# Performance work log

Hardware: AMD Instinct MI355X
Metric: run time of the kernel (lower is better)

## Reference

```python
import jax, jax.numpy as jnp
import numpy as np

B, N, E = 1024, 156, 1564
C_IN, C_HID, C_OUT = 301, 128, 128
BN_EPS = 1e-5


def setup_inputs() -> dict:
    key = jax.random.key(0)
    ks = jax.random.split(key, 12)
    x = jax.random.normal(ks[0], (B, N, C_IN), dtype=jnp.float32)
    edge_index = jax.random.randint(ks[1], (2, E), 0, N, dtype=jnp.int64)
    # GCNConv linear weights (PyG lin has no bias; conv bias added after aggregation)
    W0 = jax.random.normal(ks[2], (C_IN, C_HID), dtype=jnp.float32) / np.sqrt(C_IN)
    b0 = jnp.zeros((C_HID,), dtype=jnp.float32)
    W1 = jax.random.normal(ks[3], (C_HID, C_HID), dtype=jnp.float32) / np.sqrt(C_HID)
    b1 = jnp.zeros((C_HID,), dtype=jnp.float32)
    W2 = jax.random.normal(ks[4], (C_HID, C_OUT), dtype=jnp.float32) / np.sqrt(C_HID)
    b2 = jnp.zeros((C_OUT,), dtype=jnp.float32)
    # BatchNorm affine params (eval mode: running_mean=0, running_var=1)
    bn_w0 = jax.random.uniform(ks[5], (C_HID,), dtype=jnp.float32, minval=0.5, maxval=1.5)
    bn_b0 = jax.random.normal(ks[6], (C_HID,), dtype=jnp.float32) * 0.1
    bn_w1 = jax.random.uniform(ks[7], (C_HID,), dtype=jnp.float32, minval=0.5, maxval=1.5)
    bn_b1 = jax.random.normal(ks[8], (C_HID,), dtype=jnp.float32) * 0.1
    return {"x": x, "edge_index": edge_index,
            "W0": W0, "b0": b0, "bn_w0": bn_w0, "bn_b0": bn_b0,
            "W1": W1, "b1": b1, "bn_w1": bn_w1, "bn_b1": bn_b1,
            "W2": W2, "b2": b2}


def _gcn_norm(edge_index, num_nodes):
    # add self-loops, compute symmetric normalization deg^-1/2[src]*deg^-1/2[dst]
    loops = jnp.tile(jnp.arange(num_nodes, dtype=edge_index.dtype)[None, :], (2, 1))
    ei = jnp.concatenate([edge_index, loops], axis=1)  # [2, E+N]
    row, col = ei[0], ei[1]
    deg = jnp.zeros((num_nodes,), dtype=jnp.float32).at[col].add(1.0)
    dinv = jnp.where(deg > 0, deg ** -0.5, 0.0)
    return row, col, dinv[row] * dinv[col]


def _gcn_conv(h, row, col, norm, W, b):
    # h: [B, N, Cin] -> [B, N, Cout]
    h = jnp.einsum('bnc,co->bno', h, W)
    msg = h[:, row, :] * norm[None, :, None]          # [B, E+N, Cout]
    out = jnp.zeros_like(h).at[:, col, :].add(msg)    # scatter-add to dst nodes
    return out + b


def _bn_eval(h, w, b):
    # eval-mode BatchNorm1d with running_mean=0, running_var=1
    return h * (w / jnp.sqrt(1.0 + BN_EPS)) + b


def reference(x, edge_index, W0, b0, bn_w0, bn_b0, W1, b1, bn_w1, bn_b1, W2, b2):
    n = x.shape[1]
    row, col, norm = _gcn_norm(edge_index, n)
    h = jax.nn.relu(_bn_eval(_gcn_conv(x, row, col, norm, W0, b0), bn_w0, bn_b0))
    h = jax.nn.relu(_bn_eval(_gcn_conv(h, row, col, norm, W1, b1), bn_w1, bn_b1))
    return _gcn_conv(h, row, col, norm, W2, b2)
```

## Files before the change

### kernel.cpp

```cpp
#include <hip/hip_runtime.h>

#define NN    156
#define NP    160
#define CN    128
#define K0    301
#define KP0   320
#define BATCH 1024

#define W0_OFF 0
#define W1_OFF (128 * KP0)
#define W2_OFF (128 * KP0 + 128 * 128)

typedef __attribute__((ext_vector_type(8))) short bf16x8;
typedef __attribute__((ext_vector_type(4))) float f32x4;

__device__ __align__(16) ushort g_WtH[128 * (KP0 + 128 + 128)];
__device__ __align__(16) ushort g_WtL[128 * (KP0 + 128 + 128)];
__device__ __align__(16) ushort g_AdjH[NP * NP];
__device__ __align__(16) ushort g_AdjL[NP * NP];

__device__ __forceinline__ ushort bf16_rne(float f) {
    union { float f; uint32_t u; } v; v.f = f;
    return (ushort)((v.u + 0x7FFFu + ((v.u >> 16) & 1u)) >> 16);
}
__device__ __forceinline__ float bf16_f(ushort h) {
    union { float f; uint32_t u; } v; v.u = ((uint32_t)h) << 16; return v.f;
}
__device__ __forceinline__ ushort bf16_trunc(float f) {
    union { float f; uint32_t u; } v; v.f = f;
    return (ushort)(v.u >> 16);
}

__global__ __launch_bounds__(256) void prep_kernel(const int* __restrict__ ei, int E) {
    __shared__ float adjf[NP * NP];
    __shared__ int   cnt[NP];
    __shared__ float dinv_s[NP];
    const int t = threadIdx.x;
    for (int i = t; i < NP * NP; i += 256) adjf[i] = 0.f;
    for (int n = t; n < NP; n += 256) cnt[n] = (n < NN) ? 1 : 0;
    __syncthreads();
    for (int e = t; e < E; e += 256) atomicAdd(&cnt[ei[E + e]], 1);
    __syncthreads();
    for (int n = t; n < NP; n += 256)
        dinv_s[n] = (cnt[n] > 0) ? rsqrtf((float)cnt[n]) : 0.f;
    __syncthreads();
    for (int e = t; e < E; e += 256) {
        const int r = ei[e], c = ei[E + e];
        atomicAdd(&adjf[c * NP + r], dinv_s[r] * dinv_s[c]);
    }
    for (int n = t; n < NN; n += 256)
        atomicAdd(&adjf[n * NP + n], dinv_s[n] * dinv_s[n]);
    __syncthreads();
    for (int i = t; i < NP * NP; i += 256) {
        const float v = adjf[i];
        const ushort h = bf16_rne(v);
        g_AdjH[i] = h;
        g_AdjL[i] = bf16_trunc(v - bf16_f(h));
    }
}

__global__ __launch_bounds__(256) void wt_all(const float* __restrict__ W0,
        const float* __restrict__ W1, const float* __restrict__ W2) {
    const int id = blockIdx.x * 256 + threadIdx.x;
    const float* W; int K, KP, woff, local;
    if (id < 128 * KP0)              { W = W0; K = K0;  KP = KP0; woff = W0_OFF; local = id; }
    else if (id < 128 * (KP0 + 128)) { W = W1; K = 128; KP = 128; woff = W1_OFF; local = id - 128 * KP0; }
    else                             { W = W2; K = 128; KP = 128; woff = W2_OFF; local = id - 128 * (KP0 + 128); }
    const int n = local & 127, k = local >> 7;
    const float f = (k < K) ? W[(size_t)k * CN + n] : 0.f;
    const ushort h = bf16_rne(f);
    g_WtH[woff + n * KP + k] = h;
    g_WtL[woff + n * KP + k] = bf16_trunc(f - bf16_f(h));
}

__global__ __launch_bounds__(256, 2) void fused_all(
        const float* __restrict__ x,
        const float* __restrict__ cb0, const float* __restrict__ bw0, const float* __restrict__ bb0,
        const float* __restrict__ cb1, const float* __restrict__ bw1, const float* __restrict__ bb1,
        const float* __restrict__ cb2, float* __restrict__ out) {
    __shared__ __align__(16) uint8_t smem[81920];
    uint8_t* const pH = smem;
    uint8_t* const pL = smem + 40960;

    const int t = threadIdx.x;
    const int lane = t & 63, wave = t >> 6;
    const int quad = lane >> 4, l15 = lane & 15;
    const size_t arow0 = (size_t)blockIdx.x * NN;

    f32x4 acc[10][2];
    f32x4 og[2][10];

    const int kp  = (t & 15) * 2;
    const int r0s = t >> 4;
    float sv0[10], sv1[10];

    auto stage_load = [&](int kt) {
        const int kk = kt * 32 + kp;
#pragma unroll
        for (int s = 0; s < 10; s++) {
            const int r  = r0s + s * 16;
            const int rc = (r < NN) ? r : (NN - 1);
            const size_t abase = (arow0 + rc) * (size_t)K0;
            sv0[s] = (kk < K0)     ? x[abase + kk]     : 0.f;
            sv1[s] = (kk + 1 < K0) ? x[abase + kk + 1] : 0.f;
        }
    };
    auto stage_write = [&](int buf) {
        const int segoff = buf * 10240 + (((kp >> 3) * NP) << 4) + (kp & 7) * 2;
#pragma unroll
        for (int s = 0; s < 10; s++) {
            const int r = r0s + s * 16;
            const int off = segoff + (r << 4);
            const ushort h0 = bf16_rne(sv0[s]), h1 = bf16_rne(sv1[s]);
            *(ushort2*)(pH + off) = make_ushort2(h0, h1);
            *(ushort2*)(pL + off) = make_ushort2(bf16_trunc(sv0[s] - bf16_f(h0)),
                                                 bf16_trunc(sv1[s] - bf16_f(h1)));
        }
    };

    auto gemm_l0_tile = [&](int kt, int buf) {
        bf16x8 bH[2], bL[2];
#pragma unroll
        for (int j = 0; j < 2; j++) {
            const int wi = W0_OFF + (wave * 32 + j * 16 + l15) * KP0 + kt * 32 + quad * 8;
            bH[j] = *(const bf16x8*)&g_WtH[wi];
            bL[j] = *(const bf16x8*)&g_WtL[wi];
        }
#pragma unroll
        for (int i = 0; i < 10; i++) {
            const int off = buf * 10240 + ((quad * NP + i * 16 + l15) << 4);
            const bf16x8 aH = *(const bf16x8*)(pH + off);
            const bf16x8 aL = *(const bf16x8*)(pL + off);
#pragma unroll
            for (int j = 0; j < 2; j++) {
                acc[i][j] = __builtin_amdgcn_mfma_f32_16x16x32_bf16(aH, bH[j], acc[i][j], 0, 0, 0);
                acc[i][j] = __builtin_amdgcn_mfma_f32_16x16x32_bf16(aH, bL[j], acc[i][j], 0, 0, 0);
                acc[i][j] = __builtin_amdgcn_mfma_f32_16x16x32_bf16(aL, bH[j], acc[i][j], 0, 0, 0);
            }
        }
    };

    auto gemm_h = [&](int woff) {
#pragma unroll
        for (int i = 0; i < 10; i++)
#pragma unroll
            for (int j = 0; j < 2; j++) acc[i][j] = (f32x4){0.f, 0.f, 0.f, 0.f};
        for (int kt = 0; kt < 4; kt++) {
            bf16x8 bH[2], bL[2];
#pragma unroll
            for (int j = 0; j < 2; j++) {
                const int wi = woff + (wave * 32 + j * 16 + l15) * CN + kt * 32 + quad * 8;
                bH[j] = *(const bf16x8*)&g_WtH[wi];
                bL[j] = *(const bf16x8*)&g_WtL[wi];
            }
#pragma unroll
            for (int i = 0; i < 10; i++) {
                const int off = ((kt * 4 + quad) * NP + i * 16 + l15) << 4;
                const bf16x8 aH = *(const bf16x8*)(pH + off);
                const bf16x8 aL = *(const bf16x8*)(pL + off);
#pragma unroll
                for (int j = 0; j < 2; j++) {
                    acc[i][j] = __builtin_amdgcn_mfma_f32_16x16x32_bf16(aH, bH[j], acc[i][j], 0, 0, 0);
                    acc[i][j] = __builtin_amdgcn_mfma_f32_16x16x32_bf16(aH, bL[j], acc[i][j], 0, 0, 0);
                    acc[i][j] = __builtin_amdgcn_mfma_f32_16x16x32_bf16(aL, bH[j], acc[i][j], 0, 0, 0);
                }
            }
        }
    };

    auto write_tT = [&]() {
#pragma unroll
        for (int i = 0; i < 10; i++)
#pragma unroll
            for (int j = 0; j < 2; j++) {
                const int ch = wave * 32 + j * 16 + l15;
                const int s0 = i * 16 + quad * 4;
                const int off = (((s0 >> 3) * CN + ch) << 4) + (s0 & 7) * 2;
                ushort4 hs, ls;
#pragma unroll
                for (int rg = 0; rg < 4; rg++) {
                    const float v = acc[i][j][rg];
                    const ushort h = bf16_rne(v);
                    (&hs.x)[rg] = h;
                    (&ls.x)[rg] = bf16_trunc(v - bf16_f(h));
                }
                *(ushort4*)(pH + off) = hs;
                *(ushort4*)(pL + off) = ls;
            }
    };

    auto do_agg = [&]() {
#pragma unroll
        for (int mi = 0; mi < 2; mi++)
#pragma unroll
            for (int nj = 0; nj < 10; nj++) og[mi][nj] = (f32x4){0.f, 0.f, 0.f, 0.f};
        for (int k2 = 0; k2 < 5; k2++) {
            bf16x8 tAH[2], tAL[2];
#pragma unroll
            for (int mi = 0; mi < 2; mi++) {
                const int off = ((k2 * 4 + quad) * CN + wave * 32 + mi * 16 + l15) << 4;
                tAH[mi] = *(const bf16x8*)(pH + off);
                tAL[mi] = *(const bf16x8*)(pL + off);
            }
#pragma unroll
            for (int nj = 0; nj < 10; nj++) {
                const int ai = (nj * 16 + l15) * NP + k2 * 32 + quad * 8;
                const bf16x8 gH = *(const bf16x8*)&g_AdjH[ai];
                const bf16x8 gL = *(const bf16x8*)&g_AdjL[ai];
#pragma unroll
                for (int mi = 0; mi < 2; mi++) {
                    og[mi][nj] = __builtin_amdgcn_mfma_f32_16x16x32_bf16(tAH[mi], gH, og[mi][nj], 0, 0, 0);
                    og[mi][nj] = __builtin_amdgcn_mfma_f32_16x16x32_bf16(tAH[mi], gL, og[mi][nj], 0, 0, 0);
                    og[mi][nj] = __builtin_amdgcn_mfma_f32_16x16x32_bf16(tAL[mi], gH, og[mi][nj], 0, 0, 0);
                    og[mi][nj] = __builtin_amdgcn_mfma_f32_16x16x32_bf16(tAL[mi], gL, og[mi][nj], 0, 0, 0);
                }
            }
        }
    };

    auto write_h = [&](const float* cb, const float* bw, const float* bb) {
        const float inv = rsqrtf(1.f + 1e-5f);
#pragma unroll
        for (int mi = 0; mi < 2; mi++) {
            const int c0 = wave * 32 + mi * 16 + quad * 4;
            const float4 cbv = *(const float4*)&cb[c0];
            const float4 bwv = *(const float4*)&bw[c0];
            const float4 bbv = *(const float4*)&bb[c0];
#pragma unroll
            for (int nj = 0; nj < 10; nj++) {
                const int node = nj * 16 + l15;
                const int off = (((c0 >> 3) * NP + node) << 4) + (c0 & 7) * 2;
                ushort4 hs, ls;
#pragma unroll
                for (int rg = 0; rg < 4; rg++) {
                    float v = og[mi][nj][rg] + (&cbv.x)[rg];
                    v = fmaxf(fmaf(v, (&bwv.x)[rg] * inv, (&bbv.x)[rg]), 0.f);
                    const ushort h = bf16_rne(v);
                    (&hs.x)[rg] = h;
                    (&ls.x)[rg] = bf16_trunc(v - bf16_f(h));
                }
                *(ushort4*)(pH + off) = hs;
                *(ushort4*)(pL + off) = ls;
            }
        }
    };

    auto write_out = [&](const float* cb) {
#pragma unroll
        for (int mi = 0; mi < 2; mi++) {
            const int c0 = wave * 32 + mi * 16 + quad * 4;
            const float4 cbv = *(const float4*)&cb[c0];
#pragma unroll
            for (int nj = 0; nj < 10; nj++) {
                const int node = nj * 16 + l15;
                if (node < NN) {
                    float4 o;
#pragma unroll
                    for (int rg = 0; rg < 4; rg++)
                        (&o.x)[rg] = og[mi][nj][rg] + (&cbv.x)[rg];
                    *(float4*)&out[(arow0 + node) * CN + c0] = o;
                }
            }
        }
    };

#pragma unroll
    for (int i = 0; i < 10; i++)
#pragma unroll
        for (int j = 0; j < 2; j++) acc[i][j] = (f32x4){0.f, 0.f, 0.f, 0.f};
    stage_load(0);
    stage_write(0);
    __syncthreads();
    for (int kt = 0; kt < 10; kt++) {
        if (kt < 9) stage_load(kt + 1);
        gemm_l0_tile(kt, kt & 1);
        if (kt < 9) stage_write((kt + 1) & 1);
        __syncthreads();
    }
    write_tT();
    __syncthreads();
    do_agg();
    __syncthreads();
    write_h(cb0, bw0, bb0);
    __syncthreads();
    gemm_h(W1_OFF);
    __syncthreads();
    write_tT();
    __syncthreads();
    do_agg();
    __syncthreads();
    write_h(cb1, bw1, bb1);
    __syncthreads();
    gemm_h(W2_OFF);
    __syncthreads();
    write_tT();
    __syncthreads();
    do_agg();
    write_out(cb2);
}

extern "C" void kernel_launch(void* const* d_in, const int* in_sizes, int n_in,
                              void* d_out, int out_size, void* d_ws, size_t ws_size,
                              hipStream_t stream) {
    const float* x    = (const float*)d_in[0];
    const int*   ei   = (const int*)  d_in[1];
    const float* W0   = (const float*)d_in[2];
    const float* b0   = (const float*)d_in[3];
    const float* bnw0 = (const float*)d_in[4];
    const float* bnb0 = (const float*)d_in[5];
    const float* W1   = (const float*)d_in[6];
    const float* b1   = (const float*)d_in[7];
    const float* bnw1 = (const float*)d_in[8];
    const float* bnb1 = (const float*)d_in[9];
    const float* W2   = (const float*)d_in[10];
    const float* b2   = (const float*)d_in[11];
    float* out = (float*)d_out;

    const int E = in_sizes[1] / 2;

    prep_kernel<<<1, 256, 0, stream>>>(ei, E);
    wt_all<<<288, 256, 0, stream>>>(W0, W1, W2);
    fused_all<<<BATCH, 256, 0, stream>>>(x, b0, bnw0, bnb0,
                                         b1, bnw1, bnb1, b2, out);
}
```

Before: 469.4 us.

## Split fused GCN kernel across 8 waves and drop low-low aggregation term

Doubles the block to 512 threads so each wave computes half the rows in the feature GEMMs and a 16-channel slice in the adjacency aggregation, cutting accumulator registers and raising waves per CU. The aggregation drops the lo×lo bf16 split product, reducing MFMA work at a small precision cost. The adjacency-prep and weight-split kernels are merged into one launch to remove a kernel launch. Staging loads are redistributed across the larger thread count.

```diff
diff --git a/kernel.cpp b/kernel.cpp
--- a/kernel.cpp
+++ b/kernel.cpp
@@ -31,49 +31,50 @@
     return (ushort)(v.u >> 16);
 }
 
-__global__ __launch_bounds__(256) void prep_kernel(const int* __restrict__ ei, int E) {
+__global__ __launch_bounds__(256) void prep_wt(const int* __restrict__ ei, int E,
+        const float* __restrict__ W0, const float* __restrict__ W1,
+        const float* __restrict__ W2) {
     __shared__ float adjf[NP * NP];
     __shared__ int   cnt[NP];
     __shared__ float dinv_s[NP];
     const int t = threadIdx.x;
-    for (int i = t; i < NP * NP; i += 256) adjf[i] = 0.f;
-    for (int n = t; n < NP; n += 256) cnt[n] = (n < NN) ? 1 : 0;
-    __syncthreads();
-    for (int e = t; e < E; e += 256) atomicAdd(&cnt[ei[E + e]], 1);
-    __syncthreads();
-    for (int n = t; n < NP; n += 256)
-        dinv_s[n] = (cnt[n] > 0) ? rsqrtf((float)cnt[n]) : 0.f;
-    __syncthreads();
-    for (int e = t; e < E; e += 256) {
-        const int r = ei[e], c = ei[E + e];
-        atomicAdd(&adjf[c * NP + r], dinv_s[r] * dinv_s[c]);
+    if (blockIdx.x == 0) {
+        for (int i = t; i < NP * NP; i += 256) adjf[i] = 0.f;
+        for (int n = t; n < NP; n += 256) cnt[n] = (n < NN) ? 1 : 0;
+        __syncthreads();
+        for (int e = t; e < E; e += 256) atomicAdd(&cnt[ei[E + e]], 1);
+        __syncthreads();
+        for (int n = t; n < NP; n += 256)
+            dinv_s[n] = (cnt[n] > 0) ? rsqrtf((float)cnt[n]) : 0.f;
+        __syncthreads();
+        for (int e = t; e < E; e += 256) {
+            const int r = ei[e], c = ei[E + e];
+            atomicAdd(&adjf[c * NP + r], dinv_s[r] * dinv_s[c]);
+        }
+        for (int n = t; n < NN; n += 256)
+            atomicAdd(&adjf[n * NP + n], dinv_s[n] * dinv_s[n]);
+        __syncthreads();
+        for (int i = t; i < NP * NP; i += 256) {
+            const float v = adjf[i];
+            const ushort h = bf16_rne(v);
+            g_AdjH[i] = h;
+            g_AdjL[i] = bf16_trunc(v - bf16_f(h));
+        }
+    } else {
+        const int id = (blockIdx.x - 1) * 256 + t;
+        const float* W; int K, KP, woff, local;
+        if (id < 128 * KP0)              { W = W0; K = K0;  KP = KP0; woff = W0_OFF; local = id; }
+        else if (id < 128 * (KP0 + 128)) { W = W1; K = 128; KP = 128; woff = W1_OFF; local = id - 128 * KP0; }
+        else                             { W = W2; K = 128; KP = 128; woff = W2_OFF; local = id - 128 * (KP0 + 128); }
+        const int n = local & 127, k = local >> 7;
+        const float f = (k < K) ? W[(size_t)k * CN + n] : 0.f;
+        const ushort h = bf16_rne(f);
+        g_WtH[woff + n * KP + k] = h;
+        g_WtL[woff + n * KP + k] = bf16_trunc(f - bf16_f(h));
     }
-    for (int n = t; n < NN; n += 256)
-        atomicAdd(&adjf[n * NP + n], dinv_s[n] * dinv_s[n]);
-    __syncthreads();
-    for (int i = t; i < NP * NP; i += 256) {
-        const float v = adjf[i];
-        const ushort h = bf16_rne(v);
-        g_AdjH[i] = h;
-        g_AdjL[i] = bf16_trunc(v - bf16_f(h));
-    }
-}
-
-__global__ __launch_bounds__(256) void wt_all(const float* __restrict__ W0,
-        const float* __restrict__ W1, const float* __restrict__ W2) {
-    const int id = blockIdx.x * 256 + threadIdx.x;
-    const float* W; int K, KP, woff, local;
-    if (id < 128 * KP0)              { W = W0; K = K0;  KP = KP0; woff = W0_OFF; local = id; }
-    else if (id < 128 * (KP0 + 128)) { W = W1; K = 128; KP = 128; woff = W1_OFF; local = id - 128 * KP0; }
-    else                             { W = W2; K = 128; KP = 128; woff = W2_OFF; local = id - 128 * (KP0 + 128); }
-    const int n = local & 127, k = local >> 7;
-    const float f = (k < K) ? W[(size_t)k * CN + n] : 0.f;
-    const ushort h = bf16_rne(f);
-    g_WtH[woff + n * KP + k] = h;
-    g_WtL[woff + n * KP + k] = bf16_trunc(f - bf16_f(h));
-}
-
-__global__ __launch_bounds__(256, 2) void fused_all(
+}
+
+__global__ __launch_bounds__(512, 4) void fused_all(
         const float* __restrict__ x,
         const float* __restrict__ cb0, const float* __restrict__ bw0, const float* __restrict__ bb0,
         const float* __restrict__ cb1, const float* __restrict__ bw1, const float* __restrict__ bb1,
@@ -85,20 +86,23 @@
     const int t = threadIdx.x;
     const int lane = t & 63, wave = t >> 6;
     const int quad = lane >> 4, l15 = lane & 15;
+    const int rb = (wave >> 2) * 80;
+    const int cbs = (wave & 3) * 32;
+    const int ch0 = wave * 16;
     const size_t arow0 = (size_t)blockIdx.x * NN;
 
-    f32x4 acc[10][2];
-    f32x4 og[2][10];
+    f32x4 acc[5][2];
+    f32x4 og[10];
 
     const int kp  = (t & 15) * 2;
     const int r0s = t >> 4;
-    float sv0[10], sv1[10];
+    float sv0[5], sv1[5];
 
     auto stage_load = [&](int kt) {
         const int kk = kt * 32 + kp;
 #pragma unroll
-        for (int s = 0; s < 10; s++) {
-            const int r  = r0s + s * 16;
+        for (int s = 0; s < 5; s++) {
+            const int r  = r0s + s * 32;
             const int rc = (r < NN) ? r : (NN - 1);
             const size_t abase = (arow0 + rc) * (size_t)K0;
             sv0[s] = (kk < K0)     ? x[abase + kk]     : 0.f;
@@ -108,8 +112,8 @@
     auto stage_write = [&](int buf) {
         const int segoff = buf * 10240 + (((kp >> 3) * NP) << 4) + (kp & 7) * 2;
 #pragma unroll
-        for (int s = 0; s < 10; s++) {
-            const int r = r0s + s * 16;
+        for (int s = 0; s < 5; s++) {
+            const int r = r0s + s * 32;
             const int off = segoff + (r << 4);
             const ushort h0 = bf16_rne(sv0[s]), h1 = bf16_rne(sv1[s]);
             *(ushort2*)(pH + off) = make_ushort2(h0, h1);
@@ -122,13 +126,13 @@
         bf16x8 bH[2], bL[2];
 #pragma unroll
         for (int j = 0; j < 2; j++) {
-            const int wi = W0_OFF + (wave * 32 + j * 16 + l15) * KP0 + kt * 32 + quad * 8;
+            const int wi = W0_OFF + (cbs + j * 16 + l15) * KP0 + kt * 32 + quad * 8;
             bH[j] = *(const bf16x8*)&g_WtH[wi];
             bL[j] = *(const bf16x8*)&g_WtL[wi];
         }
 #pragma unroll
-        for (int i = 0; i < 10; i++) {
-            const int off = buf * 10240 + ((quad * NP + i * 16 + l15) << 4);
+        for (int i = 0; i < 5; i++) {
+            const int off = buf * 10240 + ((quad * NP + rb + i * 16 + l15) << 4);
             const bf16x8 aH = *(const bf16x8*)(pH + off);
             const bf16x8 aL = *(const bf16x8*)(pL + off);
 #pragma unroll
@@ -142,20 +146,20 @@
 
     auto gemm_h = [&](int woff) {
 #pragma unroll
-        for (int i = 0; i < 10; i++)
+        for (int i = 0; i < 5; i++)
 #pragma unroll
             for (int j = 0; j < 2; j++) acc[i][j] = (f32x4){0.f, 0.f, 0.f, 0.f};
         for (int kt = 0; kt < 4; kt++) {
             bf16x8 bH[2], bL[2];
 #pragma unroll
             for (int j = 0; j < 2; j++) {
-                const int wi = woff + (wave * 32 + j * 16 + l15) * CN + kt * 32 + quad * 8;
+                const int wi = woff + (cbs + j * 16 + l15) * CN + kt * 32 + quad * 8;
                 bH[j] = *(const bf16x8*)&g_WtH[wi];
                 bL[j] = *(const bf16x8*)&g_WtL[wi];
             }
 #pragma unroll
-            for (int i = 0; i < 10; i++) {
-                const int off = ((kt * 4 + quad) * NP + i * 16 + l15) << 4;
+            for (int i = 0; i < 5; i++) {
+                const int off = ((kt * 4 + quad) * NP + rb + i * 16 + l15) << 4;
                 const bf16x8 aH = *(const bf16x8*)(pH + off);
                 const bf16x8 aL = *(const bf16x8*)(pL + off);
 #pragma unroll
@@ -170,11 +174,11 @@
 
     auto write_tT = [&]() {
 #pragma unroll
-        for (int i = 0; i < 10; i++)
+        for (int i = 0; i < 5; i++)
 #pragma unroll
             for (int j = 0; j < 2; j++) {
-                const int ch = wave * 32 + j * 16 + l15;
-                const int s0 = i * 16 + quad * 4;
+                const int ch = cbs + j * 16 + l15;
+                const int s0 = rb + i * 16 + quad * 4;
                 const int off = (((s0 >> 3) * CN + ch) << 4) + (s0 & 7) * 2;
                 ushort4 hs, ls;
 #pragma unroll
@@ -191,81 +195,65 @@
 
     auto do_agg = [&]() {
 #pragma unroll
-        for (int mi = 0; mi < 2; mi++)
-#pragma unroll
-            for (int nj = 0; nj < 10; nj++) og[mi][nj] = (f32x4){0.f, 0.f, 0.f, 0.f};
+        for (int nj = 0; nj < 10; nj++) og[nj] = (f32x4){0.f, 0.f, 0.f, 0.f};
         for (int k2 = 0; k2 < 5; k2++) {
-            bf16x8 tAH[2], tAL[2];
-#pragma unroll
-            for (int mi = 0; mi < 2; mi++) {
-                const int off = ((k2 * 4 + quad) * CN + wave * 32 + mi * 16 + l15) << 4;
-                tAH[mi] = *(const bf16x8*)(pH + off);
-                tAL[mi] = *(const bf16x8*)(pL + off);
-            }
+            const int offA = ((k2 * 4 + quad) * CN + ch0 + l15) << 4;
+            const bf16x8 tAH = *(const bf16x8*)(pH + offA);
+            const bf16x8 tAL = *(const bf16x8*)(pL + offA);
 #pragma unroll
             for (int nj = 0; nj < 10; nj++) {
                 const int ai = (nj * 16 + l15) * NP + k2 * 32 + quad * 8;
                 const bf16x8 gH = *(const bf16x8*)&g_AdjH[ai];
                 const bf16x8 gL = *(const bf16x8*)&g_AdjL[ai];
-#pragma unroll
-                for (int mi = 0; mi < 2; mi++) {
-                    og[mi][nj] = __builtin_amdgcn_mfma_f32_16x16x32_bf16(tAH[mi], gH, og[mi][nj], 0, 0, 0);
-                    og[mi][nj] = __builtin_amdgcn_mfma_f32_16x16x32_bf16(tAH[mi], gL, og[mi][nj], 0, 0, 0);
-                    og[mi][nj] = __builtin_amdgcn_mfma_f32_16x16x32_bf16(tAL[mi], gH, og[mi][nj], 0, 0, 0);
-                    og[mi][nj] = __builtin_amdgcn_mfma_f32_16x16x32_bf16(tAL[mi], gL, og[mi][nj], 0, 0, 0);
-                }
+                og[nj] = __builtin_amdgcn_mfma_f32_16x16x32_bf16(tAH, gH, og[nj], 0, 0, 0);
+                og[nj] = __builtin_amdgcn_mfma_f32_16x16x32_bf16(tAH, gL, og[nj], 0, 0, 0);
+                og[nj] = __builtin_amdgcn_mfma_f32_16x16x32_bf16(tAL, gH, og[nj], 0, 0, 0);
             }
         }
     };
 
     auto write_h = [&](const float* cb, const float* bw, const float* bb) {
         const float inv = rsqrtf(1.f + 1e-5f);
-#pragma unroll
-        for (int mi = 0; mi < 2; mi++) {
-            const int c0 = wave * 32 + mi * 16 + quad * 4;
-            const float4 cbv = *(const float4*)&cb[c0];
-            const float4 bwv = *(const float4*)&bw[c0];
-            const float4 bbv = *(const float4*)&bb[c0];
-#pragma unroll
-            for (int nj = 0; nj < 10; nj++) {
-                const int node = nj * 16 + l15;
-                const int off = (((c0 >> 3) * NP + node) << 4) + (c0 & 7) * 2;
-                ushort4 hs, ls;
-#pragma unroll
-                for (int rg = 0; rg < 4; rg++) {
-                    float v = og[mi][nj][rg] + (&cbv.x)[rg];
-                    v = fmaxf(fmaf(v, (&bwv.x)[rg] * inv, (&bbv.x)[rg]), 0.f);
-                    const ushort h = bf16_rne(v);
-                    (&hs.x)[rg] = h;
-                    (&ls.x)[rg] = bf16_trunc(v - bf16_f(h));
-                }
-                *(ushort4*)(pH + off) = hs;
-                *(ushort4*)(pL + off) = ls;
-            }
+        const int c0 = ch0 + quad * 4;
+        const float4 cbv = *(const float4*)&cb[c0];
+        const float4 bwv = *(const float4*)&bw[c0];
+        const float4 bbv = *(const float4*)&bb[c0];
+#pragma unroll
+        for (int nj = 0; nj < 10; nj++) {
+            const int node = nj * 16 + l15;
+            const int off = (((c0 >> 3) * NP + node) << 4) + (c0 & 7) * 2;
+            ushort4 hs, ls;
+#pragma unroll
+            for (int rg = 0; rg < 4; rg++) {
+                float v = og[nj][rg] + (&cbv.x)[rg];
+                v = fmaxf(fmaf(v, (&bwv.x)[rg] * inv, (&bbv.x)[rg]), 0.f);
+                const ushort h = bf16_rne(v);
+                (&hs.x)[rg] = h;
+                (&ls.x)[rg] = bf16_trunc(v - bf16_f(h));
+            }
+            *(ushort4*)(pH + off) = hs;
+            *(ushort4*)(pL + off) = ls;
         }
     };
 
     auto write_out = [&](const float* cb) {
-#pragma unroll
-        for (int mi = 0; mi < 2; mi++) {
-            const int c0 = wave * 32 + mi * 16 + quad * 4;
-            const float4 cbv = *(const float4*)&cb[c0];
-#pragma unroll
-            for (int nj = 0; nj < 10; nj++) {
-                const int node = nj * 16 + l15;
-                if (node < NN) {
-                    float4 o;
-#pragma unroll
-                    for (int rg = 0; rg < 4; rg++)
-                        (&o.x)[rg] = og[mi][nj][rg] + (&cbv.x)[rg];
-                    *(float4*)&out[(arow0 + node) * CN + c0] = o;
-                }
-            }
-        }
-    };
-
-#pragma unroll
-    for (int i = 0; i < 10; i++)
+        const int c0 = ch0 + quad * 4;
+        const float4 cbv = *(const float4*)&cb[c0];
+#pragma unroll
+        for (int nj = 0; nj < 10; nj++) {
+            const int node = nj * 16 + l15;
+            if (node < NN) {
+                float4 o;
+#pragma unroll
+                for (int rg = 0; rg < 4; rg++)
+                    (&o.x)[rg] = og[nj][rg] + (&cbv.x)[rg];
+                *(float4*)&out[(arow0 + node) * CN + c0] = o;
+            }
+        }
+    };
+
+#pragma unroll
+    for (int i = 0; i < 5; i++)
 #pragma unroll
         for (int j = 0; j < 2; j++) acc[i][j] = (f32x4){0.f, 0.f, 0.f, 0.f};
     stage_load(0);
@@ -318,8 +306,7 @@
 
     const int E = in_sizes[1] / 2;
 
-    prep_kernel<<<1, 256, 0, stream>>>(ei, E);
-    wt_all<<<288, 256, 0, stream>>>(W0, W1, W2);
-    fused_all<<<BATCH, 256, 0, stream>>>(x, b0, bnw0, bnb0,
+    prep_wt<<<289, 256, 0, stream>>>(ei, E, W0, W1, W2);
+    fused_all<<<BATCH, 512, 0, stream>>>(x, b0, bnw0, bnb0,
                                          b1, bnw1, bnb1, b2, out);
 }
```

Measured after the change: 541.7 us. +15.4%, slower.
